# Performance work log

Hardware: AMD Instinct MI355X
Metric: run time of the kernel (lower is better)

## Reference

```python
import jax, jax.numpy as jnp
import numpy as np

E = 1024   # embed_dim
H = 16     # num_heads
DH = E // H
FF = 4096  # intermediate_size
EPS = 1e-5


def layernorm(x, g, b):
    mu = jnp.mean(x, axis=-1, keepdims=True)
    var = jnp.var(x, axis=-1, keepdims=True)
    return (x - mu) * jax.lax.rsqrt(var + EPS) * g + b


def setup_inputs() -> dict:
    key = jax.random.key(0)
    ks = jax.random.split(key, 16)
    s = 0.02
    return {
        "x": jax.random.normal(ks[0], (2, 2048, E), dtype=jnp.float32),
        "ln1_g": jnp.ones((E,), jnp.float32),
        "ln1_b": jnp.zeros((E,), jnp.float32),
        "ln2_g": jnp.ones((E,), jnp.float32),
        "ln2_b": jnp.zeros((E,), jnp.float32),
        # per-head Q/K/V projections stacked: [H, E, DH]
        "wq": jax.random.normal(ks[1], (H, E, DH), jnp.float32) * s,
        "bq": jnp.zeros((H, DH), jnp.float32),
        "wk": jax.random.normal(ks[2], (H, E, DH), jnp.float32) * s,
        "bk": jnp.zeros((H, DH), jnp.float32),
        "wv": jax.random.normal(ks[3], (H, E, DH), jnp.float32) * s,
        "bv": jnp.zeros((H, DH), jnp.float32),
        "wo": jax.random.normal(ks[4], (E, E), jnp.float32) * s,
        "bo": jnp.zeros((E,), jnp.float32),
        "w1": jax.random.normal(ks[5], (E, FF), jnp.float32) * s,
        "b1": jnp.zeros((FF,), jnp.float32),
        "w2": jax.random.normal(ks[6], (FF, E), jnp.float32) * s,
        "b2": jnp.zeros((E,), jnp.float32),
    }


def reference(x, ln1_g, ln1_b, ln2_g, ln2_b, wq, bq, wk, bk, wv, bv,
              wo, bo, w1, b1, w2, b2):
    # --- multi-head attention (pre-LN) ---
    h = layernorm(x, ln1_g, ln1_b)                       # [B,S,E]
    q = jnp.einsum('bse,hed->bhsd', h, wq) + bq[:, None, :]
    k = jnp.einsum('bse,hed->bhsd', h, wk) + bk[:, None, :]
    v = jnp.einsum('bse,hed->bhsd', h, wv) + bv[:, None, :]
    scores = jnp.einsum('bhsd,bhtd->bhst', q, k) / jnp.sqrt(
        jnp.asarray(DH, x.dtype))                        # [B,H,S,S]
    w = jax.nn.softmax(scores, axis=-1)
    attn = jnp.einsum('bhst,bhtd->bhsd', w, v)           # [B,H,S,DH]
    B, _, S, _ = attn.shape
    concat = attn.transpose(0, 2, 1, 3).reshape(B, S, E)  # head concat order
    x = x + concat @ wo + bo
    # --- feed-forward (pre-LN), exact GELU, dropout_p=0 ---
    h2 = layernorm(x, ln2_g, ln2_b)
    ff = jax.nn.gelu(h2 @ w1 + b1, approximate=False) @ w2 + b2
    return x + ff
```

## Files before the change

kernel.cpp:

```cpp
#include <hip/hip_runtime.h>
#include <hip/hip_bf16.h>
#include <math.h>

typedef __attribute__((ext_vector_type(8))) short short8;
typedef __attribute__((ext_vector_type(4))) float f32x4;

#define MFMA_BF16(a, b, c) __builtin_amdgcn_mfma_f32_16x16x32_bf16(a, b, c, 0, 0, 0)

#define GLD_LDS16(g, l)                                              \
  __builtin_amdgcn_global_load_lds(                                  \
      (const __attribute__((address_space(1))) void*)(g),            \
      (__attribute__((address_space(3))) void*)(l), 16, 0, 0)

__device__ __forceinline__ unsigned short f2bf(float f) {
  union { float f; unsigned u; } v; v.f = f;
  unsigned r = v.u + 0x7FFFu + ((v.u >> 16) & 1u);
  return (unsigned short)(r >> 16);
}
__device__ __forceinline__ float bf2f(unsigned short u) {
  union { unsigned u; float f; } v; v.u = ((unsigned)u) << 16;
  return v.f;
}

__global__ __launch_bounds__(256) void transpose_cast(
    const float* __restrict__ in, unsigned short* __restrict__ out,
    int R, int C, size_t in_bs, size_t out_bs) {
  __shared__ float t[32][33];
  const float* inp = in + blockIdx.z * in_bs;
  unsigned short* outp = out + blockIdx.z * out_bs;
  const int c0 = blockIdx.x * 32, r0 = blockIdx.y * 32;
  const int tx = threadIdx.x, ty = threadIdx.y;
#pragma unroll
  for (int i = 0; i < 32; i += 8)
    t[ty + i][tx] = inp[(size_t)(r0 + ty + i) * C + c0 + tx];
  __syncthreads();
#pragma unroll
  for (int i = 0; i < 32; i += 8)
    outp[(size_t)(c0 + ty + i) * R + r0 + tx] = f2bf(t[tx][ty + i]);
}

__global__ void concat_bias(const float* __restrict__ bq, const float* __restrict__ bk,
                            const float* __restrict__ bv, float* __restrict__ bcat) {
  int i = blockIdx.x * 256 + threadIdx.x;
  if (i < 1024) bcat[i] = bq[i];
  else if (i < 2048) bcat[i] = bk[i - 1024];
  else if (i < 3072) bcat[i] = bv[i - 2048];
}

__global__ __launch_bounds__(256) void ln_kernel(
    const float* __restrict__ x, const float* __restrict__ g,
    const float* __restrict__ bb, unsigned short* __restrict__ out) {
  const int row = blockIdx.x, tid = threadIdx.x;
  const float4 v = ((const float4*)(x + (size_t)row * 1024))[tid];
  float s = v.x + v.y + v.z + v.w;
  float ss = v.x * v.x + v.y * v.y + v.z * v.z + v.w * v.w;
#pragma unroll
  for (int k = 1; k < 64; k <<= 1) {
    s += __shfl_xor(s, k, 64);
    ss += __shfl_xor(ss, k, 64);
  }
  __shared__ float red[8];
  const int wid = tid >> 6;
  if ((tid & 63) == 0) { red[wid] = s; red[wid + 4] = ss; }
  __syncthreads();
  s = red[0] + red[1] + red[2] + red[3];
  ss = red[4] + red[5] + red[6] + red[7];
  const float mu = s * (1.0f / 1024.0f);
  const float var = ss * (1.0f / 1024.0f) - mu * mu;
  const float rs = rsqrtf(var + 1e-5f);
  const float4 gv = ((const float4*)g)[tid];
  const float4 bv = ((const float4*)bb)[tid];
  ushort4 o;
  o.x = f2bf((v.x - mu) * rs * gv.x + bv.x);
  o.y = f2bf((v.y - mu) * rs * gv.y + bv.y);
  o.z = f2bf((v.z - mu) * rs * gv.z + bv.z);
  o.w = f2bf((v.w - mu) * rs * gv.w + bv.w);
  ((ushort4*)(out + (size_t)row * 1024))[tid] = o;
}

template <int EPI, int BN>
__global__ __launch_bounds__(256, 2) void gemm_bt(
    const unsigned short* __restrict__ A, const unsigned short* __restrict__ Bt,
    const float* __restrict__ bias, const float* __restrict__ res,
    void* __restrict__ Cout, int M, int N, int K) {
  constexpr int NFR = BN / 32;
  __shared__ unsigned short As[4096];
  __shared__ unsigned short Bs[BN * 32];
  const int tid = threadIdx.x;
  const int wid = tid >> 6, lane = tid & 63;
  const int li = lane & 15, gi = lane >> 4;
  const int bm = blockIdx.y, bn = blockIdx.x;
  const int wr = (wid >> 1) << 6;
  const int wc = (wid & 1) * (BN / 2);

  f32x4 acc[4][NFR];
#pragma unroll
  for (int m = 0; m < 4; ++m)
#pragma unroll
    for (int n = 0; n < NFR; ++n) acc[m][n] = (f32x4)0.0f;

  const size_t Ksz = (size_t)K;
  const unsigned short* Ab = A + (size_t)(bm * 128 + (tid >> 2)) * Ksz + (tid & 3) * 8;
  const unsigned short* Bb = Bt + (size_t)(bn * BN + (tid >> 2)) * Ksz + (tid & 3) * 8;
  unsigned short* lA0 = As + wid * 512;
  unsigned short* lA1 = As + 2048 + wid * 512;
  unsigned short* lB0 = Bs + wid * 512;

  for (int kt = 0; kt < K; kt += 32) {
    GLD_LDS16(Ab + kt, lA0);
    GLD_LDS16(Ab + 64 * Ksz + kt, lA1);
    GLD_LDS16(Bb + kt, lB0);
    if (BN == 128) {
      unsigned short* lB1 = Bs + 2048 + wid * 512;
      GLD_LDS16(Bb + 64 * Ksz + kt, lB1);
    }
    __syncthreads();
    short8 af[4], bfr[NFR];
#pragma unroll
    for (int m = 0; m < 4; ++m)
      af[m] = *(const short8*)(As + (wr + m * 16 + li) * 32 + gi * 8);
#pragma unroll
    for (int n = 0; n < NFR; ++n)
      bfr[n] = *(const short8*)(Bs + (wc + n * 16 + li) * 32 + gi * 8);
#pragma unroll
    for (int m = 0; m < 4; ++m)
#pragma unroll
      for (int n = 0; n < NFR; ++n)
        acc[m][n] = MFMA_BF16(af[m], bfr[n], acc[m][n]);
    __syncthreads();
  }

  const int row_base = bm * 128 + wr + gi * 4;
  const int col_base = bn * BN + wc + li;
#pragma unroll
  for (int m = 0; m < 4; ++m) {
#pragma unroll
    for (int n = 0; n < NFR; ++n) {
      const int col = col_base + n * 16;
      const float bi = bias[col];
#pragma unroll
      for (int r = 0; r < 4; ++r) {
        const int row = row_base + m * 16 + r;
        float v = acc[m][n][r] + bi;
        if (EPI == 2) v = 0.5f * v * (1.0f + erff(v * 0.70710678118654752f));
        const size_t idx = (size_t)row * N + col;
        if (EPI == 1) ((float*)Cout)[idx] = v + res[idx];
        else ((unsigned short*)Cout)[idx] = f2bf(v);
      }
    }
  }
}

__global__ __launch_bounds__(512, 4) void attn_kernel(
    const unsigned short* __restrict__ qkv, unsigned short* __restrict__ outp) {
  __shared__ unsigned short Kl[2][4096];
  __shared__ unsigned short VsT[2][64 * 72];
  __shared__ unsigned short Pl[8][16 * 72];
  const int tid = threadIdx.x;
  const int wid = tid >> 6, lane = tid & 63;
  const int li = lane & 15, gi = lane >> 4;
  const int b = blockIdx.z, h = blockIdx.y;
  const int q0 = blockIdx.x * 128 + wid * 16;
  const int S = 2048, LD = 3072;
  const size_t base = (size_t)b * S * LD;

  short8 qa0, qa1;
  {
    const unsigned short* qrow = qkv + base + (size_t)(q0 + li) * LD + h * 64 + gi * 8;
    qa0 = *(const short8*)(qrow);
    qa1 = *(const short8*)(qrow + 32);
  }

  f32x4 o[4];
#pragma unroll
  for (int f = 0; f < 4; ++f) o[f] = (f32x4)0.0f;
  float l_[4] = {0.f, 0.f, 0.f, 0.f};

  const int krow = wid * 8 + (lane >> 3);
  const int kseg = (lane & 7) ^ ((lane >> 3) & 7);
  const unsigned short* kdma =
      qkv + base + 1024 + h * 64 + kseg * 8 + (size_t)krow * LD;

  const int vkv = lane;
  const int vd0 = wid * 8;
  const unsigned short* vsrc = qkv + base + 2048 + h * 64 + vd0 + (size_t)vkv * LD;

  auto kstage = [&](int buf, int t) {
    GLD_LDS16(kdma + (size_t)t * 64 * LD, &Kl[buf][wid * 512]);
  };
  auto vload = [&](int t) -> short8 {
    return *(const short8*)(vsrc + (size_t)t * 64 * LD);
  };
  auto vwrite = [&](int buf, short8 v) {
    unsigned short* d = &VsT[buf][0];
#pragma unroll
    for (int j = 0; j < 8; ++j) d[(vd0 + j) * 72 + vkv] = (unsigned short)v[j];
  };

  kstage(0, 0);
  vwrite(0, vload(0));
  __syncthreads();

  short8 vn{};
  for (int t = 0; t < 32; ++t) {
    if (t < 31) { vn = vload(t + 1); kstage((t + 1) & 1, t + 1); }

    const unsigned short* kl = &Kl[t & 1][0];
    short8 kb[4][2];
#pragma unroll
    for (int kvb = 0; kvb < 4; ++kvb) {
      const int row = kvb * 16 + li;
#pragma unroll
      for (int hh = 0; hh < 2; ++hh)
        kb[kvb][hh] =
            *(const short8*)(kl + row * 64 + ((gi + 4 * hh) ^ (li & 7)) * 8);
    }

    f32x4 s[4];
    __builtin_amdgcn_s_setprio(1);
#pragma unroll
    for (int kvb = 0; kvb < 4; ++kvb) {
      f32x4 z = (f32x4)0.0f;
      z = MFMA_BF16(qa0, kb[kvb][0], z);
      s[kvb] = MFMA_BF16(qa1, kb[kvb][1], z);
    }
    __builtin_amdgcn_s_setprio(0);

    unsigned short* pw = &Pl[wid][0];
#pragma unroll
    for (int kvb = 0; kvb < 4; ++kvb)
#pragma unroll
      for (int r = 0; r < 4; ++r) {
        const float p = __expf(s[kvb][r] * 0.125f);
        l_[r] += p;
        pw[(gi * 4 + r) * 72 + kvb * 16 + li] = f2bf(p);
      }
    const short8 pa0 = *(const short8*)(pw + li * 72 + gi * 8);
    const short8 pa1 = *(const short8*)(pw + li * 72 + 32 + gi * 8);

    const unsigned short* vt = &VsT[t & 1][0];
    __builtin_amdgcn_s_setprio(1);
#pragma unroll
    for (int f = 0; f < 4; ++f) {
      const int drow = (li + 16 * f) * 72;
      o[f] = MFMA_BF16(pa0, *(const short8*)(vt + drow + gi * 8), o[f]);
      o[f] = MFMA_BF16(pa1, *(const short8*)(vt + drow + 32 + gi * 8), o[f]);
    }
    __builtin_amdgcn_s_setprio(0);

    if (t < 31) vwrite((t + 1) & 1, vn);
    __syncthreads();
  }

#pragma unroll
  for (int r = 0; r < 4; ++r) {
    float u = l_[r];
    u += __shfl_xor(u, 1, 16);
    u += __shfl_xor(u, 2, 16);
    u += __shfl_xor(u, 4, 16);
    u += __shfl_xor(u, 8, 16);
    l_[r] = 1.0f / u;
  }
#pragma unroll
  for (int f = 0; f < 4; ++f)
#pragma unroll
    for (int r = 0; r < 4; ++r) {
      const int row = q0 + gi * 4 + r;
      const int col = h * 64 + li + 16 * f;
      outp[(size_t)(b * S + row) * 1024 + col] = f2bf(o[f][r] * l_[r]);
    }
}

extern "C" void kernel_launch(void* const* d_in, const int* in_sizes, int n_in,
                              void* d_out, int out_size, void* d_ws, size_t ws_size,
                              hipStream_t stream) {
  const float* x     = (const float*)d_in[0];
  const float* ln1_g = (const float*)d_in[1];
  const float* ln1_b = (const float*)d_in[2];
  const float* ln2_g = (const float*)d_in[3];
  const float* ln2_b = (const float*)d_in[4];
  const float* wq    = (const float*)d_in[5];
  const float* bq    = (const float*)d_in[6];
  const float* wk    = (const float*)d_in[7];
  const float* bk    = (const float*)d_in[8];
  const float* wv    = (const float*)d_in[9];
  const float* bv    = (const float*)d_in[10];
  const float* wo    = (const float*)d_in[11];
  const float* bo    = (const float*)d_in[12];
  const float* w1    = (const float*)d_in[13];
  const float* b1    = (const float*)d_in[14];
  const float* w2    = (const float*)d_in[15];
  const float* b2    = (const float*)d_in[16];
  float* out = (float*)d_out;

  char* p = (char*)d_ws;
  unsigned short* ws_h     = (unsigned short*)p; p += 4096ull * 1024 * 2;
  unsigned short* ws_qkv   = (unsigned short*)p; p += 4096ull * 3072 * 2;
  unsigned short* ws_attn  = (unsigned short*)p; p += 4096ull * 1024 * 2;
  unsigned short* ws_wqkvT = (unsigned short*)p; p += 3072ull * 1024 * 2;
  unsigned short* ws_woT   = (unsigned short*)p; p += 1024ull * 1024 * 2;
  unsigned short* ws_w1T   = (unsigned short*)p; p += 4096ull * 1024 * 2;
  unsigned short* ws_w2T   = (unsigned short*)p; p += 1024ull * 4096 * 2;
  float*          ws_bqkv  = (float*)p;          p += 3072 * 4;
  unsigned short* ws_ff = ws_qkv;

  const dim3 tb(32, 8);
  transpose_cast<<<dim3(2, 32, 16), tb, 0, stream>>>(
      wq, ws_wqkvT, 1024, 64, (size_t)(1024 * 64), (size_t)(64 * 1024));
  transpose_cast<<<dim3(2, 32, 16), tb, 0, stream>>>(
      wk, ws_wqkvT + 1024ull * 1024, 1024, 64, (size_t)(1024 * 64), (size_t)(64 * 1024));
  transpose_cast<<<dim3(2, 32, 16), tb, 0, stream>>>(
      wv, ws_wqkvT + 2048ull * 1024, 1024, 64, (size_t)(1024 * 64), (size_t)(64 * 1024));
  transpose_cast<<<dim3(32, 32, 1), tb, 0, stream>>>(wo, ws_woT, 1024, 1024, 0, 0);
  transpose_cast<<<dim3(128, 32, 1), tb, 0, stream>>>(w1, ws_w1T, 1024, 4096, 0, 0);
  transpose_cast<<<dim3(32, 128, 1), tb, 0, stream>>>(w2, ws_w2T, 4096, 1024, 0, 0);
  concat_bias<<<12, 256, 0, stream>>>(bq, bk, bv, ws_bqkv);

  ln_kernel<<<4096, 256, 0, stream>>>(x, ln1_g, ln1_b, ws_h);
  gemm_bt<0, 128><<<dim3(24, 32), 256, 0, stream>>>(ws_h, ws_wqkvT, ws_bqkv, nullptr,
                                                    ws_qkv, 4096, 3072, 1024);
  attn_kernel<<<dim3(16, 16, 2), 512, 0, stream>>>(ws_qkv, ws_attn);
  gemm_bt<1, 64><<<dim3(16, 32), 256, 0, stream>>>(ws_attn, ws_woT, bo, x,
                                                   out, 4096, 1024, 1024);
  ln_kernel<<<4096, 256, 0, stream>>>(out, ln2_g, ln2_b, ws_h);
  gemm_bt<2, 128><<<dim3(32, 32), 256, 0, stream>>>(ws_h, ws_w1T, b1, nullptr,
                                                    ws_ff, 4096, 4096, 1024);
  gemm_bt<1, 64><<<dim3(16, 32), 256, 0, stream>>>(ws_ff, ws_w2T, b2, out,
                                                   out, 4096, 1024, 4096);
}
```

Baseline: 290.3 us.

## Use 32x32 MFMA attention with register softmax and deepen GEMM K-tile

The attention kernel now gives each wave 32 query rows and uses 32x32x16 bf16 MFMA. It computes S^T so the probabilities can be packed in registers with cvt_pk_bf16 and permlane32_swap, instead of round-tripping through an LDS P buffer. V is staged as packed bf16 pairs in a transposed LDS tile. The GEMM doubles its K step to 64 with XOR-swizzled LDS layout and raises MFMA priority, halving barrier count per K and reducing bank conflicts. The cost is higher register pressure (launch bounds cut to 2 blocks) and fewer attention blocks in the grid.

```diff
diff --git a/kernel.cpp b/kernel.cpp
--- a/kernel.cpp
+++ b/kernel.cpp
@@ -4,22 +4,28 @@
 
 typedef __attribute__((ext_vector_type(8))) short short8;
 typedef __attribute__((ext_vector_type(4))) float f32x4;
+typedef __attribute__((ext_vector_type(16))) float f32x16;
+typedef __attribute__((ext_vector_type(4))) unsigned u32x4;
 
 #define MFMA_BF16(a, b, c) __builtin_amdgcn_mfma_f32_16x16x32_bf16(a, b, c, 0, 0, 0)
+#define MFMA32_BF16(a, b, c) __builtin_amdgcn_mfma_f32_32x32x16_bf16(a, b, c, 0, 0, 0)
 
 #define GLD_LDS16(g, l)                                              \
   __builtin_amdgcn_global_load_lds(                                  \
       (const __attribute__((address_space(1))) void*)(g),            \
       (__attribute__((address_space(3))) void*)(l), 16, 0, 0)
 
+__device__ __forceinline__ unsigned cvt_pk_bf16(float lo, float hi) {
+  unsigned r;
+  asm("v_cvt_pk_bf16_f32 %0, %1, %2" : "=v"(r) : "v"(lo), "v"(hi));
+  return r;
+}
+#define PSWAP(a, b) asm volatile("v_permlane32_swap_b32 %0, %1" : "+v"(a), "+v"(b))
+
 __device__ __forceinline__ unsigned short f2bf(float f) {
   union { float f; unsigned u; } v; v.f = f;
   unsigned r = v.u + 0x7FFFu + ((v.u >> 16) & 1u);
   return (unsigned short)(r >> 16);
-}
-__device__ __forceinline__ float bf2f(unsigned short u) {
-  union { unsigned u; float f; } v; v.u = ((unsigned)u) << 16;
-  return v.f;
 }
 
 __global__ __launch_bounds__(256) void transpose_cast(
@@ -84,8 +90,9 @@
     const float* __restrict__ bias, const float* __restrict__ res,
     void* __restrict__ Cout, int M, int N, int K) {
   constexpr int NFR = BN / 32;
-  __shared__ unsigned short As[4096];
-  __shared__ unsigned short Bs[BN * 32];
+  constexpr int BISS = BN / 32;
+  __shared__ unsigned short As[128 * 64];
+  __shared__ unsigned short Bs[BN * 64];
   const int tid = threadIdx.x;
   const int wid = tid >> 6, lane = tid & 63;
   const int li = lane & 15, gi = lane >> 4;
@@ -100,33 +107,43 @@
     for (int n = 0; n < NFR; ++n) acc[m][n] = (f32x4)0.0f;
 
   const size_t Ksz = (size_t)K;
-  const unsigned short* Ab = A + (size_t)(bm * 128 + (tid >> 2)) * Ksz + (tid & 3) * 8;
-  const unsigned short* Bb = Bt + (size_t)(bn * BN + (tid >> 2)) * Ksz + (tid & 3) * 8;
-  unsigned short* lA0 = As + wid * 512;
-  unsigned short* lA1 = As + 2048 + wid * 512;
-  unsigned short* lB0 = Bs + wid * 512;
-
-  for (int kt = 0; kt < K; kt += 32) {
-    GLD_LDS16(Ab + kt, lA0);
-    GLD_LDS16(Ab + 64 * Ksz + kt, lA1);
-    GLD_LDS16(Bb + kt, lB0);
-    if (BN == 128) {
-      unsigned short* lB1 = Bs + 2048 + wid * 512;
-      GLD_LDS16(Bb + 64 * Ksz + kt, lB1);
-    }
+  const int srow = tid >> 3;
+  const int segG = (tid & 7) ^ (srow & 7);
+  const unsigned short* Ab = A + (size_t)(bm * 128 + srow) * Ksz + segG * 8;
+  const unsigned short* Bb = Bt + (size_t)(bn * BN + srow) * Ksz + segG * 8;
+
+  for (int kt = 0; kt < K; kt += 64) {
+#pragma unroll
+    for (int c = 0; c < 4; ++c)
+      GLD_LDS16(Ab + (size_t)(c * 32) * Ksz + kt, As + c * 2048 + wid * 512);
+#pragma unroll
+    for (int c = 0; c < BISS; ++c)
+      GLD_LDS16(Bb + (size_t)(c * 32) * Ksz + kt, Bs + c * 2048 + wid * 512);
     __syncthreads();
-    short8 af[4], bfr[NFR];
+    short8 af[4][2], bf[NFR][2];
 #pragma unroll
     for (int m = 0; m < 4; ++m)
-      af[m] = *(const short8*)(As + (wr + m * 16 + li) * 32 + gi * 8);
+#pragma unroll
+      for (int kk = 0; kk < 2; ++kk) {
+        const int row = wr + m * 16 + li;
+        af[m][kk] = *(const short8*)(As + row * 64 + ((kk * 4 + gi) ^ (row & 7)) * 8);
+      }
 #pragma unroll
     for (int n = 0; n < NFR; ++n)
-      bfr[n] = *(const short8*)(Bs + (wc + n * 16 + li) * 32 + gi * 8);
+#pragma unroll
+      for (int kk = 0; kk < 2; ++kk) {
+        const int row = wc + n * 16 + li;
+        bf[n][kk] = *(const short8*)(Bs + row * 64 + ((kk * 4 + gi) ^ (row & 7)) * 8);
+      }
+    __builtin_amdgcn_s_setprio(1);
 #pragma unroll
     for (int m = 0; m < 4; ++m)
 #pragma unroll
-      for (int n = 0; n < NFR; ++n)
-        acc[m][n] = MFMA_BF16(af[m], bfr[n], acc[m][n]);
+      for (int n = 0; n < NFR; ++n) {
+        acc[m][n] = MFMA_BF16(af[m][0], bf[n][0], acc[m][n]);
+        acc[m][n] = MFMA_BF16(af[m][1], bf[n][1], acc[m][n]);
+      }
+    __builtin_amdgcn_s_setprio(0);
     __syncthreads();
   }
 
@@ -151,124 +168,127 @@
   }
 }
 
-__global__ __launch_bounds__(512, 4) void attn_kernel(
+__global__ __launch_bounds__(512, 2) void attn_kernel(
     const unsigned short* __restrict__ qkv, unsigned short* __restrict__ outp) {
   __shared__ unsigned short Kl[2][4096];
-  __shared__ unsigned short VsT[2][64 * 72];
-  __shared__ unsigned short Pl[8][16 * 72];
+  __shared__ unsigned VT[2][64 * 33];
+  __shared__ float Lb[8][32];
   const int tid = threadIdx.x;
   const int wid = tid >> 6, lane = tid & 63;
-  const int li = lane & 15, gi = lane >> 4;
+  const int l31 = lane & 31, hiq = lane >> 5;
   const int b = blockIdx.z, h = blockIdx.y;
-  const int q0 = blockIdx.x * 128 + wid * 16;
-  const int S = 2048, LD = 3072;
-  const size_t base = (size_t)b * S * LD;
-
-  short8 qa0, qa1;
+  const int q0 = blockIdx.x * 256 + wid * 32;
+  const int LD = 3072;
+  const size_t base = (size_t)b * 2048 * LD;
+
+  short8 qb[4];
   {
-    const unsigned short* qrow = qkv + base + (size_t)(q0 + li) * LD + h * 64 + gi * 8;
-    qa0 = *(const short8*)(qrow);
-    qa1 = *(const short8*)(qrow + 32);
-  }
-
-  f32x4 o[4];
-#pragma unroll
-  for (int f = 0; f < 4; ++f) o[f] = (f32x4)0.0f;
-  float l_[4] = {0.f, 0.f, 0.f, 0.f};
+    const unsigned short* qp = qkv + base + (size_t)(q0 + l31) * LD + h * 64 + hiq * 8;
+#pragma unroll
+    for (int ds = 0; ds < 4; ++ds) qb[ds] = *(const short8*)(qp + ds * 16);
+  }
+
+  f32x16 o0 = (f32x16)0.0f, o1 = (f32x16)0.0f;
+  float l_ = 0.0f;
 
   const int krow = wid * 8 + (lane >> 3);
-  const int kseg = (lane & 7) ^ ((lane >> 3) & 7);
-  const unsigned short* kdma =
-      qkv + base + 1024 + h * 64 + kseg * 8 + (size_t)krow * LD;
-
-  const int vkv = lane;
-  const int vd0 = wid * 8;
-  const unsigned short* vsrc = qkv + base + 2048 + h * 64 + vd0 + (size_t)vkv * LD;
+  const int ksegG = (lane & 7) ^ (krow & 7);
+  const unsigned short* kdma = qkv + base + 1024 + h * 64 + ksegG * 8 + (size_t)krow * LD;
+
+  const int kp = tid >> 4, dq = tid & 15;
+  const unsigned short* vsrc = qkv + base + 2048 + h * 64 + dq * 4 + (size_t)(2 * kp) * LD;
 
   auto kstage = [&](int buf, int t) {
     GLD_LDS16(kdma + (size_t)t * 64 * LD, &Kl[buf][wid * 512]);
   };
-  auto vload = [&](int t) -> short8 {
-    return *(const short8*)(vsrc + (size_t)t * 64 * LD);
-  };
-  auto vwrite = [&](int buf, short8 v) {
-    unsigned short* d = &VsT[buf][0];
-#pragma unroll
-    for (int j = 0; j < 8; ++j) d[(vd0 + j) * 72 + vkv] = (unsigned short)v[j];
-  };
 
   kstage(0, 0);
-  vwrite(0, vload(0));
+  {
+    const ushort4 a = *(const ushort4*)(vsrc);
+    const ushort4 c = *(const ushort4*)(vsrc + LD);
+    VT[0][(dq * 4 + 0) * 33 + kp] = (unsigned)a.x | ((unsigned)c.x << 16);
+    VT[0][(dq * 4 + 1) * 33 + kp] = (unsigned)a.y | ((unsigned)c.y << 16);
+    VT[0][(dq * 4 + 2) * 33 + kp] = (unsigned)a.z | ((unsigned)c.z << 16);
+    VT[0][(dq * 4 + 3) * 33 + kp] = (unsigned)a.w | ((unsigned)c.w << 16);
+  }
   __syncthreads();
 
-  short8 vn{};
   for (int t = 0; t < 32; ++t) {
-    if (t < 31) { vn = vload(t + 1); kstage((t + 1) & 1, t + 1); }
-
-    const unsigned short* kl = &Kl[t & 1][0];
-    short8 kb[4][2];
-#pragma unroll
-    for (int kvb = 0; kvb < 4; ++kvb) {
-      const int row = kvb * 16 + li;
-#pragma unroll
-      for (int hh = 0; hh < 2; ++hh)
-        kb[kvb][hh] =
-            *(const short8*)(kl + row * 64 + ((gi + 4 * hh) ^ (li & 7)) * 8);
-    }
-
-    f32x4 s[4];
+    ushort4 va{}, vc{};
+    if (t < 31) {
+      kstage((t + 1) & 1, t + 1);
+      const unsigned short* vs = vsrc + (size_t)(t + 1) * 64 * LD;
+      va = *(const ushort4*)(vs);
+      vc = *(const ushort4*)(vs + LD);
+    }
+
+    const unsigned short* kl = Kl[t & 1];
+    short8 kf[2][4];
+#pragma unroll
+    for (int kvb = 0; kvb < 2; ++kvb)
+#pragma unroll
+      for (int ds = 0; ds < 4; ++ds)
+        kf[kvb][ds] = *(const short8*)(
+            kl + (kvb * 32 + l31) * 64 + (((2 * ds + hiq) ^ (lane & 7)) * 8));
+
+    f32x16 sA = (f32x16)0.0f, sB = (f32x16)0.0f;
     __builtin_amdgcn_s_setprio(1);
 #pragma unroll
-    for (int kvb = 0; kvb < 4; ++kvb) {
-      f32x4 z = (f32x4)0.0f;
-      z = MFMA_BF16(qa0, kb[kvb][0], z);
-      s[kvb] = MFMA_BF16(qa1, kb[kvb][1], z);
+    for (int ds = 0; ds < 4; ++ds) {
+      sA = MFMA32_BF16(kf[0][ds], qb[ds], sA);
+      sB = MFMA32_BF16(kf[1][ds], qb[ds], sB);
     }
     __builtin_amdgcn_s_setprio(0);
 
-    unsigned short* pw = &Pl[wid][0];
-#pragma unroll
-    for (int kvb = 0; kvb < 4; ++kvb)
-#pragma unroll
-      for (int r = 0; r < 4; ++r) {
-        const float p = __expf(s[kvb][r] * 0.125f);
-        l_[r] += p;
-        pw[(gi * 4 + r) * 72 + kvb * 16 + li] = f2bf(p);
-      }
-    const short8 pa0 = *(const short8*)(pw + li * 72 + gi * 8);
-    const short8 pa1 = *(const short8*)(pw + li * 72 + 32 + gi * 8);
-
-    const unsigned short* vt = &VsT[t & 1][0];
-    __builtin_amdgcn_s_setprio(1);
-#pragma unroll
-    for (int f = 0; f < 4; ++f) {
-      const int drow = (li + 16 * f) * 72;
-      o[f] = MFMA_BF16(pa0, *(const short8*)(vt + drow + gi * 8), o[f]);
-      o[f] = MFMA_BF16(pa1, *(const short8*)(vt + drow + 32 + gi * 8), o[f]);
-    }
-    __builtin_amdgcn_s_setprio(0);
-
-    if (t < 31) vwrite((t + 1) & 1, vn);
+    const unsigned short* vtb = (const unsigned short*)VT[t & 1];
+#pragma unroll
+    for (int kvb = 0; kvb < 2; ++kvb) {
+      const f32x16 s = kvb ? sB : sA;
+      unsigned P[8];
+#pragma unroll
+      for (int i = 0; i < 8; ++i) {
+        const float pe = __expf(s[2 * i] * 0.125f);
+        const float po = __expf(s[2 * i + 1] * 0.125f);
+        l_ += pe + po;
+        P[i] = cvt_pk_bf16(pe, po);
+      }
+      PSWAP(P[0], P[2]); PSWAP(P[1], P[3]);
+      PSWAP(P[4], P[6]); PSWAP(P[5], P[7]);
+      const short8 pa0 = __builtin_bit_cast(short8, (u32x4){P[0], P[1], P[2], P[3]});
+      const short8 pa1 = __builtin_bit_cast(short8, (u32x4){P[4], P[5], P[6], P[7]});
+      const int ks0 = 2 * kvb;
+      const short8 v00 = *(const short8*)(vtb + (0 * 32 + l31) * 66 + (8 * ks0 + 4 * hiq) * 2);
+      const short8 v01 = *(const short8*)(vtb + (0 * 32 + l31) * 66 + (8 * ks0 + 8 + 4 * hiq) * 2);
+      const short8 v10 = *(const short8*)(vtb + (1 * 32 + l31) * 66 + (8 * ks0 + 4 * hiq) * 2);
+      const short8 v11 = *(const short8*)(vtb + (1 * 32 + l31) * 66 + (8 * ks0 + 8 + 4 * hiq) * 2);
+      __builtin_amdgcn_s_setprio(1);
+      o0 = MFMA32_BF16(pa0, v00, o0);
+      o0 = MFMA32_BF16(pa1, v01, o0);
+      o1 = MFMA32_BF16(pa0, v10, o1);
+      o1 = MFMA32_BF16(pa1, v11, o1);
+      __builtin_amdgcn_s_setprio(0);
+    }
+
+    if (t < 31) {
+      unsigned* vd = VT[(t + 1) & 1];
+      vd[(dq * 4 + 0) * 33 + kp] = (unsigned)va.x | ((unsigned)vc.x << 16);
+      vd[(dq * 4 + 1) * 33 + kp] = (unsigned)va.y | ((unsigned)vc.y << 16);
+      vd[(dq * 4 + 2) * 33 + kp] = (unsigned)va.z | ((unsigned)vc.z << 16);
+      vd[(dq * 4 + 3) * 33 + kp] = (unsigned)va.w | ((unsigned)vc.w << 16);
+    }
     __syncthreads();
   }
 
-#pragma unroll
-  for (int r = 0; r < 4; ++r) {
-    float u = l_[r];
-    u += __shfl_xor(u, 1, 16);
-    u += __shfl_xor(u, 2, 16);
-    u += __shfl_xor(u, 4, 16);
-    u += __shfl_xor(u, 8, 16);
-    l_[r] = 1.0f / u;
-  }
-#pragma unroll
-  for (int f = 0; f < 4; ++f)
-#pragma unroll
-    for (int r = 0; r < 4; ++r) {
-      const int row = q0 + gi * 4 + r;
-      const int col = h * 64 + li + 16 * f;
-      outp[(size_t)(b * S + row) * 1024 + col] = f2bf(o[f][r] * l_[r]);
-    }
+  const float lt = l_ + __shfl_xor(l_, 32, 64);
+  Lb[wid][l31] = 1.0f / lt;
+#pragma unroll
+  for (int r = 0; r < 16; ++r) {
+    const int crow = (r & 3) + 8 * (r >> 2) + 4 * hiq;
+    const float inv = Lb[wid][crow];
+    const size_t rowb = (size_t)(b * 2048 + q0 + crow) * 1024 + h * 64 + l31;
+    outp[rowb]      = f2bf(o0[r] * inv);
+    outp[rowb + 32] = f2bf(o1[r] * inv);
+  }
 }
 
 extern "C" void kernel_launch(void* const* d_in, const int* in_sizes, int n_in,
@@ -319,7 +339,7 @@
   ln_kernel<<<4096, 256, 0, stream>>>(x, ln1_g, ln1_b, ws_h);
   gemm_bt<0, 128><<<dim3(24, 32), 256, 0, stream>>>(ws_h, ws_wqkvT, ws_bqkv, nullptr,
                                                     ws_qkv, 4096, 3072, 1024);
-  attn_kernel<<<dim3(16, 16, 2), 512, 0, stream>>>(ws_qkv, ws_attn);
+  attn_kernel<<<dim3(8, 16, 2), 512, 0, stream>>>(ws_qkv, ws_attn);
   gemm_bt<1, 64><<<dim3(16, 32), 256, 0, stream>>>(ws_attn, ws_woT, bo, x,
                                                    out, 4096, 1024, 1024);
   ln_kernel<<<4096, 256, 0, stream>>>(out, ln2_g, ln2_b, ws_h);
```

After: 290.6 us. No clear change (+0.1%).
